# Kernel tuning notes

Hardware: AMD Instinct MI355X
Metric: run time of the kernel (lower is better)

The kernel has to match this reference:

```python
import jax, jax.numpy as jnp
import numpy as np
from functools import partial

GAMMA = 1.0
LAM = 1.0
N_ITER = 60  # fixed iteration count for the projected-gradient dual fused-lasso solver
GROUP_TOL = 1e-6


def _gfl_solve_row(x, A, lam):
    """Graph fused lasso: argmin_y 0.5||y-x||^2 + lam*sum_ij A_ij |y_i - y_j|.
    Solved by projected gradient ascent on the dual (edge flows z_ij in [-lam*A_ij, lam*A_ij]).
    x: [N], A: [N, N] -> y: [N]
    """
    N = x.shape[0]
    w = lam * A
    step = jnp.asarray(1.0 / (2.0 * N), dtype=x.dtype)

    def body(z, _):
        y = x - jnp.sum(z, axis=1) + jnp.sum(z, axis=0)  # primal from flows
        z = jnp.clip(z + step * (y[:, None] - y[None, :]), -w, w)
        return z, None

    z, _ = jax.lax.scan(body, jnp.zeros_like(A), None, length=N_ITER)
    return x - jnp.sum(z, axis=1) + jnp.sum(z, axis=0)


@partial(jax.custom_vjp, nondiff_argnums=(2,))
def gfusedlasso(x, A, lam):
    # x: [B, N], A: [B, N, N]
    return jax.vmap(_gfl_solve_row, in_axes=(0, 0, None))(x, A, lam)


def _gfl_fwd(x, A, lam):
    out = gfusedlasso(x, A, lam)
    return out, out


def _gfl_bwd(lam, out, g):
    # Faithful to backward_gfusedmax_torch_1D: average grad over groups of equal outputs.
    eq = (jnp.abs(out[:, :, None] - out[:, None, :]) < GROUP_TOL).astype(g.dtype)  # [B,N,N]
    grad_x = jnp.einsum('bij,bj->bi', eq, g) / jnp.sum(eq, axis=2)
    return grad_x, jnp.zeros_like(eq)  # no gradient defined for A (matches torch)


gfusedlasso.defvjp(_gfl_fwd, _gfl_bwd)


def sparsemax(x, axis=-1):
    # torch_sparsemax.forward with gamma=1.0
    N = x.shape[axis]
    x_sorted = jnp.flip(jnp.sort(x, axis=axis), axis=axis)  # descending
    cumsum = jnp.cumsum(x_sorted, axis=axis)
    k = jnp.arange(1, N + 1, dtype=x.dtype)  # broadcast along last axis
    mask = (1.0 + k * x_sorted > cumsum).astype(x.dtype)
    tau = (jnp.sum(x_sorted * mask, axis=axis, keepdims=True) - 1.0) / jnp.sum(mask, axis=axis, keepdims=True)
    return jnp.maximum(x - tau, 0.0)


def setup_inputs() -> dict:
    key = jax.random.key(0)
    kx, ka = jax.random.split(key)
    B, N = 4096, 128
    x = jax.random.normal(kx, (B, N), dtype=jnp.float32)
    A = jax.random.uniform(ka, (B, N, N), dtype=jnp.float32)
    return {"x": x, "A": A}


def reference(x, A):
    # Gfusedmax.forward: x/gamma -> gfusedlasso(lam/gamma) -> sparsemax(gamma=1)
    xg = x / GAMMA
    fused = gfusedlasso(xg, A, LAM / GAMMA)
    return sparsemax(fused, axis=-1)
```

## Files before the change

kernel.cpp:

```cpp
#include <hip/hip_runtime.h>

#define N 128
#define NITER 60
#define PST 132
#define COLOFF 2128

typedef float v2f __attribute__((ext_vector_type(2)));
typedef float v4f __attribute__((ext_vector_type(4)));

__global__ __launch_bounds__(256, 1)
void gfusedmax_kernel(const float* __restrict__ x,
                      const float* __restrict__ A,
                      float* __restrict__ out)
{
    const int b   = blockIdx.x;
    const int tid = threadIdx.x;
    const int tr  = tid >> 4;
    const int tc  = tid & 15;
    const int i0  = tr * 8;
    const int j0  = tc * 8;

    __shared__ __align__(16) float parts[COLOFF + 16 * PST];
    __shared__ __align__(16) float yv[N];
    __shared__ float sorted[N];
    __shared__ float red[8];

    const float step = 1.0f / 256.0f;

    v2f w2[8][4];
    v2f z2[8][4];
    const float* Ab = A + (size_t)b * N * N;
    #pragma unroll
    for (int r = 0; r < 8; ++r) {
        const v4f* src = (const v4f*)(Ab + (size_t)(i0 + r) * N + j0);
        v4f p0 = src[0];
        v4f p1 = src[1];
        w2[r][0] = p0.lo; w2[r][1] = p0.hi;
        w2[r][2] = p1.lo; w2[r][3] = p1.hi;
        #pragma unroll
        for (int cp = 0; cp < 4; ++cp) z2[r][cp] = (v2f)0.0f;
    }

    const int m = tid >> 1;
    const float xm = x[(size_t)b * N + m];
    const float* pb = parts + ((tid & 1) ? COLOFF : 0);

    v2f pr2[8], pc2[4];
    #pragma unroll
    for (int r = 0; r < 8; ++r) pr2[r] = (v2f)0.0f;
    #pragma unroll
    for (int cp = 0; cp < 4; ++cp) pc2[cp] = (v2f)0.0f;

    for (int it = 0; it <= NITER; ++it) {
        v4f r0, r1, c0, c1;
        r0.x = pr2[0].x + pr2[0].y;  r0.y = pr2[1].x + pr2[1].y;
        r0.z = pr2[2].x + pr2[2].y;  r0.w = pr2[3].x + pr2[3].y;
        r1.x = pr2[4].x + pr2[4].y;  r1.y = pr2[5].x + pr2[5].y;
        r1.z = pr2[6].x + pr2[6].y;  r1.w = pr2[7].x + pr2[7].y;
        c0.x = pc2[0].x; c0.y = pc2[0].y; c0.z = pc2[1].x; c0.w = pc2[1].y;
        c1.x = pc2[2].x; c1.y = pc2[2].y; c1.z = pc2[3].x; c1.w = pc2[3].y;
        *(v4f*)&parts[tc * PST + i0]              = r0;
        *(v4f*)&parts[tc * PST + i0 + 4]          = r1;
        *(v4f*)&parts[COLOFF + tr * PST + j0]     = c0;
        *(v4f*)&parts[COLOFF + tr * PST + j0 + 4] = c1;
        __syncthreads();

        float acc = 0.0f;
        #pragma unroll
        for (int k = 0; k < 16; ++k) acc += pb[k * PST + m];
        float other = __shfl_xor(acc, 1, 64);
        if (!(tid & 1)) {
            float y = (xm - acc) + other;
            yv[m] = (it == NITER) ? y : step * y;
        }
        __syncthreads();
        if (it == NITER) break;

        v2f drs[8], ec2[4];
        #pragma unroll
        for (int r = 0; r < 8; ++r) drs[r] = (v2f)yv[i0 + r];
        v4f e0 = *(const v4f*)&yv[j0];
        v4f e1 = *(const v4f*)&yv[j0 + 4];
        ec2[0] = e0.lo; ec2[1] = e0.hi;
        ec2[2] = e1.lo; ec2[3] = e1.hi;
        #pragma unroll
        for (int r = 0; r < 8; ++r) {
            #pragma unroll
            for (int cp = 0; cp < 4; ++cp) {
                v2f t  = (z2[r][cp] + drs[r]) - ec2[cp];
                v2f wv = w2[r][cp];
                v2f zn;
                zn.x = __builtin_amdgcn_fmed3f(t.x, -wv.x, wv.x);
                zn.y = __builtin_amdgcn_fmed3f(t.y, -wv.y, wv.y);
                z2[r][cp] = zn;
                pr2[r]  = (cp == 0) ? zn : pr2[r] + zn;
                pc2[cp] = (r == 0)  ? zn : pc2[cp] + zn;
            }
        }
    }

    float v = 0.0f;
    if (tid < N) {
        v = yv[tid];
        int rk = 0;
        for (int k = 0; k < N; ++k) {
            float u = yv[k];
            rk += (u > v) || (u == v && k < tid);
        }
        sorted[rk] = v;
    }
    __syncthreads();

    float s = 0.0f, csum = 0.0f;
    if (tid < N) {
        s = sorted[tid];
        for (int mm = 0; mm < N; ++mm) {
            float t = sorted[mm];
            if (mm <= tid) csum += t;
        }
    }
    bool mask = (tid < N) && (1.0f + (float)(tid + 1) * s > csum);
    float aRed = mask ? s : 0.0f;
    float bRed = mask ? 1.0f : 0.0f;
    #pragma unroll
    for (int off = 32; off >= 1; off >>= 1) {
        aRed += __shfl_down(aRed, off, 64);
        bRed += __shfl_down(bRed, off, 64);
    }
    const int wid = tid >> 6;
    if ((tid & 63) == 0) { red[wid * 2] = aRed; red[wid * 2 + 1] = bRed; }
    __syncthreads();
    const float tau = (red[0] + red[2] + red[4] + red[6] - 1.0f)
                    / (red[1] + red[3] + red[5] + red[7]);
    if (tid < N) out[(size_t)b * N + tid] = fmaxf(v - tau, 0.0f);
}

extern "C" void kernel_launch(void* const* d_in, const int* in_sizes, int n_in,
                              void* d_out, int out_size, void* d_ws, size_t ws_size,
                              hipStream_t stream) {
    const float* x = (const float*)d_in[0];
    const float* A = (const float*)d_in[1];
    float* out = (float*)d_out;
    const int B = in_sizes[0] / N;
    gfusedmax_kernel<<<B, 256, 0, stream>>>(x, A, out);
}
```

Before: 826.7 us.

## Pack two rows per block and ping-pong update/reduce phases between groups

Each block now handles two batch rows with 512 threads. The two 256-thread groups alternate phases: one does the clipped flow update while the other reduces partial sums into y. The per-iteration loop is also restructured so the update writes its row and column partials directly, and y is initialized from x. The aim is to fill the barrier-separated idle phases with useful work from the other row. The cost is larger shared memory per block and a launch-bounds change that may pressure registers.

After: 1.012 ms. 22.4% more time.

```diff
diff --git a/kernel.cpp b/kernel.cpp
--- a/kernel.cpp
+++ b/kernel.cpp
@@ -4,32 +4,35 @@
 #define NITER 60
 #define PST 132
 #define COLOFF 2128
+#define GBUF (COLOFF + 16 * PST)
 
 typedef float v2f __attribute__((ext_vector_type(2)));
 typedef float v4f __attribute__((ext_vector_type(4)));
 
-__global__ __launch_bounds__(256, 1)
+__global__ __launch_bounds__(512, 2)
 void gfusedmax_kernel(const float* __restrict__ x,
                       const float* __restrict__ A,
                       float* __restrict__ out)
 {
-    const int b   = blockIdx.x;
     const int tid = threadIdx.x;
-    const int tr  = tid >> 4;
-    const int tc  = tid & 15;
+    const int grp = tid >> 8;
+    const int lt  = tid & 255;
+    const int tr  = lt >> 4;
+    const int tc  = lt & 15;
     const int i0  = tr * 8;
     const int j0  = tc * 8;
+    const int row = blockIdx.x * 2 + grp;
 
-    __shared__ __align__(16) float parts[COLOFF + 16 * PST];
-    __shared__ __align__(16) float yv[N];
-    __shared__ float sorted[N];
-    __shared__ float red[8];
+    __shared__ __align__(16) float parts[2][GBUF];
+    __shared__ __align__(16) float yv[2][N];
+    __shared__ float sorted[2][N];
+    __shared__ float red[2][8];
 
     const float step = 1.0f / 256.0f;
 
     v2f w2[8][4];
     v2f z2[8][4];
-    const float* Ab = A + (size_t)b * N * N;
+    const float* Ab = A + (size_t)row * N * N;
     #pragma unroll
     for (int r = 0; r < 8; ++r) {
         const v4f* src = (const v4f*)(Ab + (size_t)(i0 + r) * N + j0);
@@ -41,48 +44,23 @@
         for (int cp = 0; cp < 4; ++cp) z2[r][cp] = (v2f)0.0f;
     }
 
-    const int m = tid >> 1;
-    const float xm = x[(size_t)b * N + m];
-    const float* pb = parts + ((tid & 1) ? COLOFF : 0);
+    const int m = lt >> 1;
+    const float xm = x[(size_t)row * N + m];
+    const float* pb = &parts[grp][0] + ((lt & 1) ? COLOFF : 0);
+    float* yvg = yv[grp];
 
-    v2f pr2[8], pc2[4];
-    #pragma unroll
-    for (int r = 0; r < 8; ++r) pr2[r] = (v2f)0.0f;
-    #pragma unroll
-    for (int cp = 0; cp < 4; ++cp) pc2[cp] = (v2f)0.0f;
+    if (lt < N) yvg[lt] = step * x[(size_t)row * N + lt];
+    __syncthreads();
 
-    for (int it = 0; it <= NITER; ++it) {
-        v4f r0, r1, c0, c1;
-        r0.x = pr2[0].x + pr2[0].y;  r0.y = pr2[1].x + pr2[1].y;
-        r0.z = pr2[2].x + pr2[2].y;  r0.w = pr2[3].x + pr2[3].y;
-        r1.x = pr2[4].x + pr2[4].y;  r1.y = pr2[5].x + pr2[5].y;
-        r1.z = pr2[6].x + pr2[6].y;  r1.w = pr2[7].x + pr2[7].y;
-        c0.x = pc2[0].x; c0.y = pc2[0].y; c0.z = pc2[1].x; c0.w = pc2[1].y;
-        c1.x = pc2[2].x; c1.y = pc2[2].y; c1.z = pc2[3].x; c1.w = pc2[3].y;
-        *(v4f*)&parts[tc * PST + i0]              = r0;
-        *(v4f*)&parts[tc * PST + i0 + 4]          = r1;
-        *(v4f*)&parts[COLOFF + tr * PST + j0]     = c0;
-        *(v4f*)&parts[COLOFF + tr * PST + j0 + 4] = c1;
-        __syncthreads();
-
-        float acc = 0.0f;
-        #pragma unroll
-        for (int k = 0; k < 16; ++k) acc += pb[k * PST + m];
-        float other = __shfl_xor(acc, 1, 64);
-        if (!(tid & 1)) {
-            float y = (xm - acc) + other;
-            yv[m] = (it == NITER) ? y : step * y;
-        }
-        __syncthreads();
-        if (it == NITER) break;
-
+    auto UPDATE = [&]() {
         v2f drs[8], ec2[4];
         #pragma unroll
-        for (int r = 0; r < 8; ++r) drs[r] = (v2f)yv[i0 + r];
-        v4f e0 = *(const v4f*)&yv[j0];
-        v4f e1 = *(const v4f*)&yv[j0 + 4];
+        for (int r = 0; r < 8; ++r) drs[r] = (v2f)yvg[i0 + r];
+        v4f e0 = *(const v4f*)&yvg[j0];
+        v4f e1 = *(const v4f*)&yvg[j0 + 4];
         ec2[0] = e0.lo; ec2[1] = e0.hi;
         ec2[2] = e1.lo; ec2[3] = e1.hi;
+        v2f pr2[8], pc2[4];
         #pragma unroll
         for (int r = 0; r < 8; ++r) {
             #pragma unroll
@@ -97,42 +75,75 @@
                 pc2[cp] = (r == 0)  ? zn : pc2[cp] + zn;
             }
         }
+        v4f r0, r1, c0, c1;
+        r0.x = pr2[0].x + pr2[0].y;  r0.y = pr2[1].x + pr2[1].y;
+        r0.z = pr2[2].x + pr2[2].y;  r0.w = pr2[3].x + pr2[3].y;
+        r1.x = pr2[4].x + pr2[4].y;  r1.y = pr2[5].x + pr2[5].y;
+        r1.z = pr2[6].x + pr2[6].y;  r1.w = pr2[7].x + pr2[7].y;
+        c0.x = pc2[0].x; c0.y = pc2[0].y; c0.z = pc2[1].x; c0.w = pc2[1].y;
+        c1.x = pc2[2].x; c1.y = pc2[2].y; c1.z = pc2[3].x; c1.w = pc2[3].y;
+        *(v4f*)&parts[grp][tc * PST + i0]              = r0;
+        *(v4f*)&parts[grp][tc * PST + i0 + 4]          = r1;
+        *(v4f*)&parts[grp][COLOFF + tr * PST + j0]     = c0;
+        *(v4f*)&parts[grp][COLOFF + tr * PST + j0 + 4] = c1;
+    };
+
+    auto REDUCE = [&](bool raw) {
+        float acc = 0.0f;
+        #pragma unroll
+        for (int k = 0; k < 16; ++k) acc += pb[k * PST + m];
+        float other = __shfl_xor(acc, 1, 64);
+        if (!(lt & 1)) {
+            float y = (xm - acc) + other;
+            yvg[m] = raw ? y : step * y;
+        }
+    };
+
+    for (int t = 0; t <= NITER; ++t) {
+        if (grp == 0) { if (t < NITER) UPDATE(); }
+        else          { if (t > 0) REDUCE(t == NITER); }
+        __syncthreads();
+        if (t == NITER) break;
+        if (grp == 1) UPDATE();
+        else          REDUCE(t == NITER - 1);
+        __syncthreads();
     }
 
+    float* sog = sorted[grp];
     float v = 0.0f;
-    if (tid < N) {
-        v = yv[tid];
+    if (lt < N) {
+        v = yvg[lt];
         int rk = 0;
         for (int k = 0; k < N; ++k) {
-            float u = yv[k];
-            rk += (u > v) || (u == v && k < tid);
+            float u = yvg[k];
+            rk += (u > v) || (u == v && k < lt);
         }
-        sorted[rk] = v;
+        sog[rk] = v;
     }
     __syncthreads();
 
     float s = 0.0f, csum = 0.0f;
-    if (tid < N) {
-        s = sorted[tid];
+    if (lt < N) {
+        s = sog[lt];
         for (int mm = 0; mm < N; ++mm) {
-            float t = sorted[mm];
-            if (mm <= tid) csum += t;
+            float u = sog[mm];
+            if (mm <= lt) csum += u;
         }
     }
-    bool mask = (tid < N) && (1.0f + (float)(tid + 1) * s > csum);
-    float aRed = mask ? s : 0.0f;
-    float bRed = mask ? 1.0f : 0.0f;
+    bool maskb = (lt < N) && (1.0f + (float)(lt + 1) * s > csum);
+    float aRed = maskb ? s : 0.0f;
+    float bRed = maskb ? 1.0f : 0.0f;
     #pragma unroll
     for (int off = 32; off >= 1; off >>= 1) {
         aRed += __shfl_down(aRed, off, 64);
         bRed += __shfl_down(bRed, off, 64);
     }
-    const int wid = tid >> 6;
-    if ((tid & 63) == 0) { red[wid * 2] = aRed; red[wid * 2 + 1] = bRed; }
+    const int wid = lt >> 6;
+    if ((lt & 63) == 0) { red[grp][wid * 2] = aRed; red[grp][wid * 2 + 1] = bRed; }
     __syncthreads();
-    const float tau = (red[0] + red[2] + red[4] + red[6] - 1.0f)
-                    / (red[1] + red[3] + red[5] + red[7]);
-    if (tid < N) out[(size_t)b * N + tid] = fmaxf(v - tau, 0.0f);
+    const float tau = (red[grp][0] + red[grp][2] + red[grp][4] + red[grp][6] - 1.0f)
+                    / (red[grp][1] + red[grp][3] + red[grp][5] + red[grp][7]);
+    if (lt < N) out[(size_t)row * N + lt] = fmaxf(v - tau, 0.0f);
 }
 
 extern "C" void kernel_launch(void* const* d_in, const int* in_sizes, int n_in,
@@ -142,5 +153,5 @@
     const float* A = (const float*)d_in[1];
     float* out = (float*)d_out;
     const int B = in_sizes[0] / N;
-    gfusedmax_kernel<<<B, 256, 0, stream>>>(x, A, out);
+    gfusedmax_kernel<<<B / 2, 512, 0, stream>>>(x, A, out);
 }
```
